# Optimization experiments

Hardware: AMD Instinct MI355X
Metric: run time of the kernel (lower is better)

## Reference

```python
import jax, jax.numpy as jnp
import numpy as np


def _chamfer_one(x, y):
    # x: [N,3], y: [M,3]; squared-Euclidean pairwise distances via norm expansion
    x2 = jnp.sum(x * x, axis=-1)  # [N]
    y2 = jnp.sum(y * y, axis=-1)  # [M]
    cross = jnp.einsum('nd,md->nm', x, y)  # [N,M]
    d = x2[:, None] + y2[None, :] - 2.0 * cross  # [N,M] squared distances
    # kaolin chamfer_distance: mean of NN sq-dists in both directions, summed (w1=w2=1)
    return jnp.mean(jnp.min(d, axis=1)) + jnp.mean(jnp.min(d, axis=0))


def reference(x, y):
    # x, y: [B, N, 3] / [B, M, 3]
    per_sample = jax.vmap(_chamfer_one)(x, y)  # [B]
    return jnp.mean(per_sample)


def setup_inputs() -> dict:
    key = jax.random.key(0)
    kx, ky = jax.random.split(key)
    x = jax.random.normal(kx, (16, 4096, 3), dtype=jnp.float32)
    y = jax.random.normal(ky, (16, 4096, 3), dtype=jnp.float32)
    return {"x": x, "y": y}
```

## Files before the change

### kernel.cpp

```cpp
#include <hip/hip_runtime.h>
#include <hip/hip_fp16.h>
#include <math.h>


typedef _Float16 f16x8  __attribute__((ext_vector_type(8)));
typedef float    f32x16 __attribute__((ext_vector_type(16)));

constexpr int BATCH = 16;
constexpr int NPTS  = 4096;
constexpr int NDB   = 2 * BATCH;
constexpr int BN    = BATCH * NPTS;
constexpr int NROW  = NDB * NPTS;
constexpr int TCH   = 4;
constexpr int TPC   = NPTS / TCH;
constexpr int TILES = TPC / 32;

__global__ void __launch_bounds__(256)
prep(const float* __restrict__ x, const float* __restrict__ y,
     f16x8* __restrict__ ta, f16x8* __restrict__ qb, float* __restrict__ out) {
    int i = blockIdx.x * 256 + threadIdx.x;
    if (i == 0) out[0] = 0.0f;
    if (i >= 2 * BN) return;
    int src = i >> 16;
    int rem = i & (BN - 1);
    const float* S = src ? y : x;
    float a = S[3 * rem], b = S[3 * rem + 1], c = S[3 * rem + 2];
    _Float16 ha = (_Float16)a, hb = (_Float16)b, hc = (_Float16)c;
    float fa = (float)ha, fb = (float)hb, fc = (float)hc;
    float ss = fa * fa + fb * fb + fc * fc;
    _Float16 shi = (_Float16)ss;
    _Float16 slo = (_Float16)(ss - (float)shi);
    const _Float16 one = (_Float16)1.0f, zz = (_Float16)0.0f;
    f16x8 t = { (_Float16)(-2.0f * fa), (_Float16)(-2.0f * fb),
                (_Float16)(-2.0f * fc), shi, slo, one, one, zz };
    f16x8 q = { ha, hb, hc, one, one, shi, slo, zz };
    ta[(1 - src) * BN + rem] = t;
    qb[src       * BN + rem] = q;
}

__global__ void __launch_bounds__(256, 4)
chamfer_mfma(const f16x8* __restrict__ ta, const f16x8* __restrict__ qb,
             float* __restrict__ rowpart) {
    const int bid  = blockIdx.x;
    const int tch  = bid & (TCH - 1);
    const int qgrp = (bid >> 2) & 31;
    const int db   = bid >> 7;
    const int lane = threadIdx.x & 63;
    const int wave = threadIdx.x >> 6;
    const int m    = lane & 31;
    const bool lower = lane < 32;

    const f16x8 zero8 = { (_Float16)0.0f, (_Float16)0.0f, (_Float16)0.0f,
                          (_Float16)0.0f, (_Float16)0.0f, (_Float16)0.0f,
                          (_Float16)0.0f, (_Float16)0.0f };

    const int qtile = qgrp * 4 + wave;
    f16x8 braw  = qb[(size_t)db * NPTS + qtile * 32 + m];
    f16x8 bfrag = lower ? braw : zero8;

    const f16x8* tptr = ta + (size_t)db * NPTS + tch * TPC;
    const f32x16 z = {0.0f, 0.0f, 0.0f, 0.0f, 0.0f, 0.0f, 0.0f, 0.0f,
                      0.0f, 0.0f, 0.0f, 0.0f, 0.0f, 0.0f, 0.0f, 0.0f};
    float acc = INFINITY;

    #pragma unroll 2
    for (int tt = 0; tt < TILES; ++tt) {
        f16x8 araw = tptr[tt * 32 + m];
        f16x8 af   = lower ? araw : zero8;
        f32x16 d = __builtin_amdgcn_mfma_f32_32x32x16_f16(af, bfrag, z, 0, 0, 0);
        float m0 = fminf(fminf(d[0],  d[1]),  fminf(d[2],  d[3]));
        float m1 = fminf(fminf(d[4],  d[5]),  fminf(d[6],  d[7]));
        float m2 = fminf(fminf(d[8],  d[9]),  fminf(d[10], d[11]));
        float m3 = fminf(fminf(d[12], d[13]), fminf(d[14], d[15]));
        acc = fminf(acc, fminf(fminf(m0, m1), fminf(m2, m3)));
    }

    acc = fminf(acc, __shfl_xor(acc, 32, 64));
    if (lower)
        rowpart[(size_t)tch * NROW + db * NPTS + qtile * 32 + m] = acc;
}

__global__ void __launch_bounds__(256)
finalize(const float* __restrict__ rowpart, float* __restrict__ out) {
    const int n4 = NROW / 4;
    float s = 0.0f;
    for (int i = blockIdx.x * 256 + threadIdx.x; i < n4;
         i += gridDim.x * 256) {
        float4 a = *(const float4*)(rowpart + 0 * (size_t)NROW + 4 * i);
        float4 b = *(const float4*)(rowpart + 1 * (size_t)NROW + 4 * i);
        float4 c = *(const float4*)(rowpart + 2 * (size_t)NROW + 4 * i);
        float4 d = *(const float4*)(rowpart + 3 * (size_t)NROW + 4 * i);
        float mx = fminf(fminf(a.x, b.x), fminf(c.x, d.x));
        float my = fminf(fminf(a.y, b.y), fminf(c.y, d.y));
        float mz = fminf(fminf(a.z, b.z), fminf(c.z, d.z));
        float mw = fminf(fminf(a.w, b.w), fminf(c.w, d.w));
        s += (mx + my) + (mz + mw);
    }
    #pragma unroll
    for (int off = 32; off > 0; off >>= 1) s += __shfl_down(s, off, 64);
    __shared__ float ws_s[4];
    if ((threadIdx.x & 63) == 0) ws_s[threadIdx.x >> 6] = s;
    __syncthreads();
    if (threadIdx.x == 0) {
        float b = ws_s[0] + ws_s[1] + ws_s[2] + ws_s[3];
        atomicAdd(out, b * (1.0f / ((float)BATCH * (float)NPTS)));
    }
}

extern "C" void kernel_launch(void* const* d_in, const int* in_sizes, int n_in,
                              void* d_out, int out_size, void* d_ws, size_t ws_size,
                              hipStream_t stream) {
    const float* x = (const float*)d_in[0];
    const float* y = (const float*)d_in[1];
    float* out = (float*)d_out;

    const size_t npt = (size_t)NDB * NPTS;
    f16x8* ta = (f16x8*)d_ws;
    f16x8* qb = ta + npt;
    float* rowpart = (float*)(qb + npt);

    hipLaunchKernelGGL(prep, dim3((2 * BN + 255) / 256), dim3(256), 0, stream,
                       x, y, ta, qb, out);
    hipLaunchKernelGGL(chamfer_mfma, dim3(NDB * 32 * TCH), dim3(256), 0,
                       stream, ta, qb, rowpart);
    hipLaunchKernelGGL(finalize, dim3(64), dim3(256), 0, stream,
                       rowpart, out);
}
```

Before: 87.56 us.

## Fuse finalize into chamfer kernel, drop target chunking, prepad zero fragments

The separate finalize kernel and the rowpart buffer are removed. Each block now scans all target tiles and reduces its row minima straight into the output with a wave shuffle-sum and one atomic per block. The prep kernel writes zero-padded 64-entry fragments, so the main loop loads them directly instead of selecting by lane. This saves one launch and the partial-result round trip through memory, but the grid shrinks four-fold (1024 blocks) and each block runs a longer serial loop, which may reduce parallelism. It also doubles the workspace the prep stage writes.

```diff
diff --git a/kernel.cpp b/kernel.cpp
--- a/kernel.cpp
+++ b/kernel.cpp
@@ -10,10 +10,8 @@
 constexpr int NPTS  = 4096;
 constexpr int NDB   = 2 * BATCH;
 constexpr int BN    = BATCH * NPTS;
-constexpr int NROW  = NDB * NPTS;
-constexpr int TCH   = 4;
-constexpr int TPC   = NPTS / TCH;
-constexpr int TILES = TPC / 32;
+constexpr int TILES = NPTS / 32;
+constexpr int EPDB  = TILES * 64;
 
 __global__ void __launch_bounds__(256)
 prep(const float* __restrict__ x, const float* __restrict__ y,
@@ -21,8 +19,10 @@
     int i = blockIdx.x * 256 + threadIdx.x;
     if (i == 0) out[0] = 0.0f;
     if (i >= 2 * BN) return;
-    int src = i >> 16;
-    int rem = i & (BN - 1);
+    int src   = i >> 16;
+    int rem   = i & (BN - 1);
+    int batch = rem >> 12;
+    int p     = rem & (NPTS - 1);
     const float* S = src ? y : x;
     float a = S[3 * rem], b = S[3 * rem + 1], c = S[3 * rem + 2];
     _Float16 ha = (_Float16)a, hb = (_Float16)b, hc = (_Float16)c;
@@ -31,42 +31,39 @@
     _Float16 shi = (_Float16)ss;
     _Float16 slo = (_Float16)(ss - (float)shi);
     const _Float16 one = (_Float16)1.0f, zz = (_Float16)0.0f;
+    f16x8 zero8 = { zz, zz, zz, zz, zz, zz, zz, zz };
     f16x8 t = { (_Float16)(-2.0f * fa), (_Float16)(-2.0f * fb),
                 (_Float16)(-2.0f * fc), shi, slo, one, one, zz };
     f16x8 q = { ha, hb, hc, one, one, shi, slo, zz };
-    ta[(1 - src) * BN + rem] = t;
-    qb[src       * BN + rem] = q;
+    int db_t = (1 - src) * BATCH + batch;
+    int db_q = src * BATCH + batch;
+    size_t slot = (size_t)(p >> 5) * 64 + (p & 31);
+    ta[(size_t)db_t * EPDB + slot]      = t;
+    ta[(size_t)db_t * EPDB + slot + 32] = zero8;
+    qb[(size_t)db_q * EPDB + slot]      = q;
+    qb[(size_t)db_q * EPDB + slot + 32] = zero8;
 }
 
 __global__ void __launch_bounds__(256, 4)
 chamfer_mfma(const f16x8* __restrict__ ta, const f16x8* __restrict__ qb,
-             float* __restrict__ rowpart) {
+             float* __restrict__ out) {
     const int bid  = blockIdx.x;
-    const int tch  = bid & (TCH - 1);
-    const int qgrp = (bid >> 2) & 31;
-    const int db   = bid >> 7;
+    const int qgrp = bid & 31;
+    const int db   = bid >> 5;
     const int lane = threadIdx.x & 63;
     const int wave = threadIdx.x >> 6;
-    const int m    = lane & 31;
-    const bool lower = lane < 32;
-
-    const f16x8 zero8 = { (_Float16)0.0f, (_Float16)0.0f, (_Float16)0.0f,
-                          (_Float16)0.0f, (_Float16)0.0f, (_Float16)0.0f,
-                          (_Float16)0.0f, (_Float16)0.0f };
 
     const int qtile = qgrp * 4 + wave;
-    f16x8 braw  = qb[(size_t)db * NPTS + qtile * 32 + m];
-    f16x8 bfrag = lower ? braw : zero8;
+    const f16x8 bfrag = qb[(size_t)db * EPDB + qtile * 64 + lane];
+    const f16x8* abase = ta + (size_t)db * EPDB;
 
-    const f16x8* tptr = ta + (size_t)db * NPTS + tch * TPC;
     const f32x16 z = {0.0f, 0.0f, 0.0f, 0.0f, 0.0f, 0.0f, 0.0f, 0.0f,
                       0.0f, 0.0f, 0.0f, 0.0f, 0.0f, 0.0f, 0.0f, 0.0f};
     float acc = INFINITY;
 
     #pragma unroll 2
     for (int tt = 0; tt < TILES; ++tt) {
-        f16x8 araw = tptr[tt * 32 + m];
-        f16x8 af   = lower ? araw : zero8;
+        f16x8 af = abase[tt * 64 + lane];
         f32x16 d = __builtin_amdgcn_mfma_f32_32x32x16_f16(af, bfrag, z, 0, 0, 0);
         float m0 = fminf(fminf(d[0],  d[1]),  fminf(d[2],  d[3]));
         float m1 = fminf(fminf(d[4],  d[5]),  fminf(d[6],  d[7]));
@@ -76,34 +73,15 @@
     }
 
     acc = fminf(acc, __shfl_xor(acc, 32, 64));
-    if (lower)
-        rowpart[(size_t)tch * NROW + db * NPTS + qtile * 32 + m] = acc;
-}
+    #pragma unroll
+    for (int off = 1; off < 64; off <<= 1) acc += __shfl_xor(acc, off, 64);
 
-__global__ void __launch_bounds__(256)
-finalize(const float* __restrict__ rowpart, float* __restrict__ out) {
-    const int n4 = NROW / 4;
-    float s = 0.0f;
-    for (int i = blockIdx.x * 256 + threadIdx.x; i < n4;
-         i += gridDim.x * 256) {
-        float4 a = *(const float4*)(rowpart + 0 * (size_t)NROW + 4 * i);
-        float4 b = *(const float4*)(rowpart + 1 * (size_t)NROW + 4 * i);
-        float4 c = *(const float4*)(rowpart + 2 * (size_t)NROW + 4 * i);
-        float4 d = *(const float4*)(rowpart + 3 * (size_t)NROW + 4 * i);
-        float mx = fminf(fminf(a.x, b.x), fminf(c.x, d.x));
-        float my = fminf(fminf(a.y, b.y), fminf(c.y, d.y));
-        float mz = fminf(fminf(a.z, b.z), fminf(c.z, d.z));
-        float mw = fminf(fminf(a.w, b.w), fminf(c.w, d.w));
-        s += (mx + my) + (mz + mw);
-    }
-    #pragma unroll
-    for (int off = 32; off > 0; off >>= 1) s += __shfl_down(s, off, 64);
-    __shared__ float ws_s[4];
-    if ((threadIdx.x & 63) == 0) ws_s[threadIdx.x >> 6] = s;
+    __shared__ float s4[4];
+    if (lane == 0) s4[wave] = acc;
     __syncthreads();
     if (threadIdx.x == 0) {
-        float b = ws_s[0] + ws_s[1] + ws_s[2] + ws_s[3];
-        atomicAdd(out, b * (1.0f / ((float)BATCH * (float)NPTS)));
+        float b = (s4[0] + s4[1]) + (s4[2] + s4[3]);
+        atomicAdd(out, b * (0.5f / ((float)BATCH * (float)NPTS)));
     }
 }
 
@@ -114,15 +92,11 @@
     const float* y = (const float*)d_in[1];
     float* out = (float*)d_out;
 
-    const size_t npt = (size_t)NDB * NPTS;
     f16x8* ta = (f16x8*)d_ws;
-    f16x8* qb = ta + npt;
-    float* rowpart = (float*)(qb + npt);
+    f16x8* qb = ta + (size_t)NDB * EPDB;
 
     hipLaunchKernelGGL(prep, dim3((2 * BN + 255) / 256), dim3(256), 0, stream,
                        x, y, ta, qb, out);
-    hipLaunchKernelGGL(chamfer_mfma, dim3(NDB * 32 * TCH), dim3(256), 0,
-                       stream, ta, qb, rowpart);
-    hipLaunchKernelGGL(finalize, dim3(64), dim3(256), 0, stream,
-                       rowpart, out);
+    hipLaunchKernelGGL(chamfer_mfma, dim3(NDB * 32), dim3(256), 0, stream,
+                       ta, qb, out);
 }
```

Result: slower. 96.42 us (+10.1%).
